# Performance work log

Hardware: AMD Instinct MI355X
Metric: run time of the kernel (lower is better)

Reference implementation:

```python
import jax, jax.numpy as jnp
import numpy as np

NP, NA = 200000, 100000        # paper / author node counts
EW, EC = 300000, 300000        # writes / cites edge counts
HID, H, D = 128, 4, 32         # hidden, heads, head dim
FIN_P, FIN_A, OUT = 256, 128, 16
SCALE = float(1.0 / np.sqrt(D))


def _seg_softmax(alpha, idx, n):
    # softmax over edges grouped by destination node (PyG softmax)
    m = jax.ops.segment_max(alpha, idx, num_segments=n)
    e = jnp.exp(alpha - m[idx])
    s = jax.ops.segment_sum(e, idx, num_segments=n)
    return e / (s[idx] + 1e-16)


def _edge_type(k_src, v_src, q_dst, src, dst, a_rel, m_rel, p_rel, n_dst):
    # per-relation transform at node level, then gather-attend-scatter
    kr = jnp.einsum('nhd,hde->nhe', k_src, a_rel)
    vr = jnp.einsum('nhd,hde->nhe', v_src, m_rel)
    alpha = jnp.sum(q_dst[dst] * kr[src], axis=-1) * p_rel * SCALE  # [E,H]
    alpha = _seg_softmax(alpha, dst, n_dst)
    return jax.ops.segment_sum(vr[src] * alpha[..., None], dst, num_segments=n_dst)


def setup_inputs() -> dict:
    key = jax.random.key(0)
    ks = iter(jax.random.split(key, 48))

    def nrm(shape, s=0.05):
        return jax.random.normal(next(ks), shape, jnp.float32) * s

    inp = dict(
        x_paper=nrm((NP, FIN_P), 1.0),
        x_author=nrm((NA, FIN_A), 1.0),
        writes_src=jax.random.randint(next(ks), (EW,), 0, NA, dtype=jnp.int32),
        writes_dst=jax.random.randint(next(ks), (EW,), 0, NP, dtype=jnp.int32),
        cites_src=jax.random.randint(next(ks), (EC,), 0, NP, dtype=jnp.int32),
        cites_dst=jax.random.randint(next(ks), (EC,), 0, NP, dtype=jnp.int32),
        lin_paper_w=nrm((FIN_P, HID)), lin_paper_b=jnp.zeros((HID,), jnp.float32),
        lin_author_w=nrm((FIN_A, HID)), lin_author_b=jnp.zeros((HID,), jnp.float32),
        lin_out_w=nrm((HID, OUT)), lin_out_b=jnp.zeros((OUT,), jnp.float32),
    )
    for t in ('paper', 'author'):
        for nm in ('k', 'q', 'v', 'a'):
            inp[f'{nm}_w_{t}'] = nrm((HID, HID))
            inp[f'{nm}_b_{t}'] = jnp.zeros((HID,), jnp.float32)
        inp[f'skip_{t}'] = jnp.ones((), jnp.float32)
    for e in ('writes', 'cites'):
        inp[f'a_rel_{e}'] = nrm((H, D, D), 0.18)
        inp[f'm_rel_{e}'] = nrm((H, D, D), 0.18)
        inp[f'p_rel_{e}'] = jnp.ones((H,), jnp.float32)
    return inp


def reference(x_paper, x_author, writes_src, writes_dst, cites_src, cites_dst,
              lin_paper_w, lin_paper_b, lin_author_w, lin_author_b,
              lin_out_w, lin_out_b,
              k_w_paper, k_b_paper, q_w_paper, q_b_paper, v_w_paper, v_b_paper,
              a_w_paper, a_b_paper, skip_paper,
              k_w_author, k_b_author, q_w_author, q_b_author, v_w_author, v_b_author,
              a_w_author, a_b_author, skip_author,
              a_rel_writes, m_rel_writes, p_rel_writes,
              a_rel_cites, m_rel_cites, p_rel_cites):
    # per-node-type input projection + relu
    hp = jax.nn.relu(x_paper @ lin_paper_w + lin_paper_b)
    ha = jax.nn.relu(x_author @ lin_author_w + lin_author_b)
    # HGTConv: per-node-type k/q/v, [N,H,D]
    k_p = (hp @ k_w_paper + k_b_paper).reshape(NP, H, D)
    q_p = (hp @ q_w_paper + q_b_paper).reshape(NP, H, D)
    v_p = (hp @ v_w_paper + v_b_paper).reshape(NP, H, D)
    k_a = (ha @ k_w_author + k_b_author).reshape(NA, H, D)
    v_a = (ha @ v_w_author + v_b_author).reshape(NA, H, D)
    # heterogeneous multi-relation attention, group='sum' over edge types
    out_p = _edge_type(k_a, v_a, q_p, writes_src, writes_dst,
                       a_rel_writes, m_rel_writes, p_rel_writes, NP)
    out_p = out_p + _edge_type(k_p, v_p, q_p, cites_src, cites_dst,
                               a_rel_cites, m_rel_cites, p_rel_cites, NP)
    # output projection + gated skip (paper type; only 'paper' feeds the head)
    op = jax.nn.gelu(out_p.reshape(NP, HID), approximate=False) @ a_w_paper + a_b_paper
    beta = jax.nn.sigmoid(skip_paper)
    hp = beta * op + (1.0 - beta) * hp
    return hp @ lin_out_w + lin_out_b  # [NP, OUT]
```

## Files before the change

kernel.cpp:

```cpp
#include <hip/hip_runtime.h>
#include <cstdint>

#define NP 200000
#define NA 100000
#define EW 300000
#define EC 300000
#define HID 128
#define FIN_P 256
#define FIN_A 128
#define NOUT 16
#define ATT_SCALE 0.17677669529663687f

#define NBP 1563
#define NBA 782

#define SCAN_N (2 * NP)
#define SCAN_BS 256
#define SCAN_ITEMS 4
#define SCAN_TILE 1024
#define SCAN_NB ((SCAN_N + SCAN_TILE - 1) / SCAN_TILE)

typedef short s8v __attribute__((ext_vector_type(8)));
typedef float f32x4 __attribute__((ext_vector_type(4)));
typedef unsigned short ushort_t;

__device__ __forceinline__ float gelu_f(float x) {
  return 0.5f * x * (1.0f + erff(x * 0.70710678118654752f));
}
__device__ __forceinline__ ushort_t f2bf(float f) {
  unsigned u = __float_as_uint(f);
  return (ushort_t)((u + 0x7FFFu + ((u >> 16) & 1u)) >> 16);
}
__device__ __forceinline__ unsigned pack2bf(float a, float b) {
  return (unsigned)f2bf(a) | ((unsigned)f2bf(b) << 16);
}
__device__ __forceinline__ unsigned cvtpk(float a, float b) {
  unsigned r;
  asm("v_cvt_pk_bf16_f32 %0, %1, %2" : "=v"(r) : "v"(a), "v"(b));
  return r;
}
__device__ __forceinline__ float bflo(unsigned u) { return __uint_as_float(u << 16); }
__device__ __forceinline__ float bfhi(unsigned u) { return __uint_as_float(u & 0xFFFF0000u); }

__device__ __forceinline__ void gl16(const void* g, void* l) {
  __builtin_amdgcn_global_load_lds(
      (const __attribute__((address_space(1))) void*)g,
      (__attribute__((address_space(3))) void*)l, 16, 0, 0);
}

__device__ __forceinline__ int s2row(int r) { return (r ^ (r >> 2)) & 3; }

__global__ void prep_all(
    const float* __restrict__ qw,  const float* __restrict__ qb,
    const float* __restrict__ kwp, const float* __restrict__ kbp, const float* __restrict__ arc,
    const float* __restrict__ vwp, const float* __restrict__ vbp, const float* __restrict__ mrc,
    const float* __restrict__ kwa, const float* __restrict__ kba, const float* __restrict__ arw,
    const float* __restrict__ vwa, const float* __restrict__ vba, const float* __restrict__ mrw,
    const float* __restrict__ lpw, const float* __restrict__ law,
    const float* __restrict__ aw, const float* __restrict__ ab,
    const float* __restrict__ skip, const float* __restrict__ W2, const float* __restrict__ b2,
    ushort_t* __restrict__ Wall, float* __restrict__ Ball,
    ushort_t* __restrict__ Wcatb, float* __restrict__ bo,
    int* __restrict__ cnt)
{
  const int b = blockIdx.x, tid = threadIdx.x;
  if (b == 0) {
    for (int idx = tid; idx < 16384; idx += 256) {
      int c = idx >> 7, r = idx & 127;
      Wall[idx] = f2bf(qw[r * 128 + c]);
    }
    for (int c = tid; c < 128; c += 256) Ball[c] = qb[c];
  } else if (b <= 4) {
    const float *W, *bias, *rel;
    switch (b) {
      case 1:  W = kwp; bias = kbp; rel = arc; break;
      case 2:  W = vwp; bias = vbp; rel = mrc; break;
      case 3:  W = kwa; bias = kba; rel = arw; break;
      default: W = vwa; bias = vba; rel = mrw; break;
    }
    for (int idx = tid; idx < 16384; idx += 256) {
      int c = idx >> 7, r = idx & 127, h = c >> 5, e = c & 31;
      float s = 0.f;
      #pragma unroll
      for (int d = 0; d < 32; ++d) s += W[r * 128 + h * 32 + d] * rel[h * 1024 + d * 32 + e];
      Wall[b * 16384 + idx] = f2bf(s);
    }
    for (int c = tid; c < 128; c += 256) {
      int h = c >> 5, e = c & 31;
      float s = 0.f;
      #pragma unroll
      for (int d = 0; d < 32; ++d) s += bias[h * 32 + d] * rel[h * 1024 + d * 32 + e];
      Ball[b * 128 + c] = s;
    }
  } else if (b == 5) {
    for (int idx = tid; idx < 16384; idx += 256) {
      int c = idx >> 7, r = idx & 127;
      Wall[5 * 16384 + idx] = f2bf(law[r * 128 + c]);
    }
  } else if (b == 6) {
    for (int idx = tid; idx < 32768; idx += 256) {
      int c = idx >> 8, r = idx & 255;
      Wall[6 * 16384 + idx] = f2bf(lpw[r * 128 + c]);
    }
  } else if (b == 7) {
    float beta = 1.0f / (1.0f + expf(-skip[0]));
    for (int idx = tid; idx < 4096; idx += 256) {
      int c = idx >> 8, k = idx & 255;
      float v;
      if (k < 128) {
        float s = 0.f;
        for (int j = 0; j < 128; ++j) s += aw[k * 128 + j] * W2[j * 16 + c];
        v = beta * s;
      } else {
        v = (1.0f - beta) * W2[(k - 128) * 16 + c];
      }
      Wcatb[c * 256 + k] = f2bf(v);
    }
    if (tid < 16) {
      float s = 0.f;
      for (int k = 0; k < 128; ++k) s += ab[k] * W2[k * 16 + tid];
      bo[tid] = beta * s + b2[tid];
    }
  } else {
    int chunk = SCAN_N / 8;
    int base = (b - 8) * chunk;
    for (int i = tid; i < chunk; i += 256) cnt[base + i] = 0;
  }
}

__global__ __launch_bounds__(256, 1) void gemm_proj(
    const float* __restrict__ xp, const float* __restrict__ xa,
    const ushort_t* __restrict__ Wall,
    const float* __restrict__ bp, const float* __restrict__ ba,
    ushort_t* __restrict__ hpo, ushort_t* __restrict__ hao)
{
  __shared__ ushort_t As[8192];
  __shared__ ushort_t Bs[8192];
  const bool isP = blockIdx.x < NBP;
  const int bid = isP ? blockIdx.x : blockIdx.x - NBP;
  const float* A = isP ? xp : xa;
  const ushort_t* W = Wall + (isP ? 6 * 16384 : 5 * 16384);
  const float* bias = isP ? bp : ba;
  ushort_t* C = isP ? hpo : hao;
  const int M = isP ? NP : NA;
  const int KT = isP ? 256 : 128;
  const int nt = KT >> 6;

  const int tid  = threadIdx.x;
  const int lane = tid & 63;
  const int wv   = tid >> 6;
  const int wr   = wv >> 1, wc = wv & 1;
  const int l15  = lane & 15, kgl = lane >> 4;
  const int s2l  = (l15 ^ (l15 >> 2)) & 3;
  const int row0 = bid * 128;

  const int r0 = tid >> 2, kgp = tid & 3;
  const int sk = kgp ^ s2row(r0);
  int g0 = row0 + r0;       if (g0 > M - 1) g0 = M - 1;
  int g1 = row0 + r0 + 64;  if (g1 > M - 1) g1 = M - 1;
  const float* a0p = A + (size_t)g0 * KT + sk * 8;
  const float* a1p = A + (size_t)g1 * KT + sk * 8;
  const ushort_t* b0p = W + (size_t)r0 * KT + sk * 8;
  const ushort_t* b1p = W + (size_t)(r0 + 64) * KT + sk * 8;

  f32x4 acc[4][4];
  #pragma unroll
  for (int i = 0; i < 4; ++i)
    #pragma unroll
    for (int j = 0; j < 4; ++j) acc[i][j] = (f32x4){0.f, 0.f, 0.f, 0.f};

  for (int t = 0; t < nt; ++t) {
    const int kt = t * 64;
    gl16(b0p + kt,      &Bs[(size_t)tid * 8]);
    gl16(b1p + kt,      &Bs[(size_t)(tid + 256) * 8]);
    gl16(b0p + kt + 32, &Bs[(size_t)(tid + 512) * 8]);
    gl16(b1p + kt + 32, &Bs[(size_t)(tid + 768) * 8]);
    float4 fa0 = *(const float4*)(a0p + kt);
    float4 fa1 = *(const float4*)(a0p + kt + 4);
    float4 fa2 = *(const float4*)(a1p + kt);
    float4 fa3 = *(const float4*)(a1p + kt + 4);
    float4 fb0 = *(const float4*)(a0p + kt + 32);
    float4 fb1 = *(const float4*)(a0p + kt + 36);
    float4 fb2 = *(const float4*)(a1p + kt + 32);
    float4 fb3 = *(const float4*)(a1p + kt + 36);
    uint4 v;
    v.x = cvtpk(fa0.x, fa0.y); v.y = cvtpk(fa0.z, fa0.w);
    v.z = cvtpk(fa1.x, fa1.y); v.w = cvtpk(fa1.z, fa1.w);
    *(uint4*)&As[(size_t)tid * 8] = v;
    v.x = cvtpk(fa2.x, fa2.y); v.y = cvtpk(fa2.z, fa2.w);
    v.z = cvtpk(fa3.x, fa3.y); v.w = cvtpk(fa3.z, fa3.w);
    *(uint4*)&As[(size_t)(tid + 256) * 8] = v;
    v.x = cvtpk(fb0.x, fb0.y); v.y = cvtpk(fb0.z, fb0.w);
    v.z = cvtpk(fb1.x, fb1.y); v.w = cvtpk(fb1.z, fb1.w);
    *(uint4*)&As[(size_t)(tid + 512) * 8] = v;
    v.x = cvtpk(fb2.x, fb2.y); v.y = cvtpk(fb2.z, fb2.w);
    v.z = cvtpk(fb3.x, fb3.y); v.w = cvtpk(fb3.z, fb3.w);
    *(uint4*)&As[(size_t)(tid + 768) * 8] = v;
    __syncthreads();

    const s8v* As8 = (const s8v*)As;
    const s8v* Bs8 = (const s8v*)Bs;
    #pragma unroll
    for (int pg = 0; pg < 2; ++pg) {
      s8v af[4], bfv[4];
      #pragma unroll
      for (int i = 0; i < 4; ++i)
        af[i]  = As8[pg * 512 + (wr * 64 + i * 16 + l15) * 4 + (kgl ^ s2l)];
      #pragma unroll
      for (int j = 0; j < 4; ++j)
        bfv[j] = Bs8[pg * 512 + (wc * 64 + j * 16 + l15) * 4 + (kgl ^ s2l)];
      #pragma unroll
      for (int i = 0; i < 4; ++i)
        #pragma unroll
        for (int j = 0; j < 4; ++j)
          acc[i][j] = __builtin_amdgcn_mfma_f32_16x16x32_bf16(af[i], bfv[j], acc[i][j], 0, 0, 0);
    }
    __syncthreads();
  }

  float bv[4];
  #pragma unroll
  for (int j = 0; j < 4; ++j) bv[j] = bias[wc * 64 + j * 16 + l15];
  #pragma unroll
  for (int i = 0; i < 4; ++i) {
    #pragma unroll
    for (int r = 0; r < 4; ++r) {
      int row = row0 + wr * 64 + i * 16 + kgl * 4 + r;
      if (row < M) {
        #pragma unroll
        for (int j = 0; j < 4; ++j) {
          float vv = acc[i][j][r] + bv[j];
          vv = fmaxf(vv, 0.f);
          C[(size_t)row * 128 + wc * 64 + j * 16 + l15] = f2bf(vv);
        }
      }
    }
  }
}

__global__ __launch_bounds__(256) void gemm_kv(
    const ushort_t* __restrict__ hpA, const ushort_t* __restrict__ haA,
    const ushort_t* __restrict__ Wall, const float* __restrict__ Ball,
    ushort_t* __restrict__ qkv, ushort_t* __restrict__ kvw)
{
  __shared__ ushort_t As[16384];
  __shared__ ushort_t Bs[16384];
  const bool isP = blockIdx.x < NBP;
  const int bid = isP ? blockIdx.x : blockIdx.x - NBP;
  const ushort_t* A = isP ? hpA : haA;
  const int M = isP ? NP : NA;
  const int base_set = isP ? 0 : 3;
  const int nsets = isP ? 3 : 2;

  const int tid  = threadIdx.x;
  const int lane = tid & 63;
  const int wv   = tid >> 6;
  const int wr   = wv >> 1, wc = wv & 1;
  const int l15  = lane & 15, kgl = lane >> 4;
  const int s2l  = (l15 ^ (l15 >> 2)) & 3;
  const int row0 = bid * 128;

  const int r0 = tid >> 2, kgp = tid & 3;
  const int sk = kgp ^ s2row(r0);
  int g0 = row0 + r0;       if (g0 > M - 1) g0 = M - 1;
  int g1 = row0 + r0 + 64;  if (g1 > M - 1) g1 = M - 1;
  const ushort_t* a0p = A + (size_t)g0 * 128 + sk * 8;
  const ushort_t* a1p = A + (size_t)g1 * 128 + sk * 8;

  #pragma unroll
  for (int t = 0; t < 4; ++t) {
    gl16(a0p + t * 32, &As[((size_t)t * 512 + tid) * 8]);
    gl16(a1p + t * 32, &As[((size_t)t * 512 + tid + 256) * 8]);
  }

  for (int si = 0; si < nsets; ++si) {
    const int set = base_set + si;
    const ushort_t* W = Wall + set * 16384;
    const float* bias = Ball + set * 128;
    ushort_t* C = isP ? (qkv + (size_t)set * NP * HID)
                      : (kvw + (size_t)(set - 3) * NA * HID);
    const ushort_t* b0p = W + (size_t)r0 * 128 + sk * 8;
    const ushort_t* b1p = W + (size_t)(r0 + 64) * 128 + sk * 8;
    #pragma unroll
    for (int t = 0; t < 4; ++t) {
      gl16(b0p + t * 32, &Bs[((size_t)t * 512 + tid) * 8]);
      gl16(b1p + t * 32, &Bs[((size_t)t * 512 + tid + 256) * 8]);
    }
    __syncthreads();

    f32x4 acc[4][4];
    #pragma unroll
    for (int i = 0; i < 4; ++i)
      #pragma unroll
      for (int j = 0; j < 4; ++j) acc[i][j] = (f32x4){0.f, 0.f, 0.f, 0.f};

    const s8v* As8 = (const s8v*)As;
    const s8v* Bs8 = (const s8v*)Bs;
    #pragma unroll
    for (int t = 0; t < 4; ++t) {
      s8v af[4], bfv[4];
      #pragma unroll
      for (int i = 0; i < 4; ++i)
        af[i]  = As8[t * 512 + (wr * 64 + i * 16 + l15) * 4 + (kgl ^ s2l)];
      #pragma unroll
      for (int j = 0; j < 4; ++j)
        bfv[j] = Bs8[t * 512 + (wc * 64 + j * 16 + l15) * 4 + (kgl ^ s2l)];
      #pragma unroll
      for (int i = 0; i < 4; ++i)
        #pragma unroll
        for (int j = 0; j < 4; ++j)
          acc[i][j] = __builtin_amdgcn_mfma_f32_16x16x32_bf16(af[i], bfv[j], acc[i][j], 0, 0, 0);
    }

    float bv[4];
    #pragma unroll
    for (int j = 0; j < 4; ++j) bv[j] = bias[wc * 64 + j * 16 + l15];
    #pragma unroll
    for (int i = 0; i < 4; ++i) {
      #pragma unroll
      for (int r = 0; r < 4; ++r) {
        int row = row0 + wr * 64 + i * 16 + kgl * 4 + r;
        if (row < M) {
          #pragma unroll
          for (int j = 0; j < 4; ++j) {
            C[(size_t)row * 128 + wc * 64 + j * 16 + l15] = f2bf(acc[i][j][r] + bv[j]);
          }
        }
      }
    }
    __syncthreads();
  }
}

__global__ void hist_k(const int* __restrict__ wdst, const int* __restrict__ cdst,
                       int* __restrict__ cnt)
{
  int t = blockIdx.x * blockDim.x + threadIdx.x;
  if (t < EW) atomicAdd(&cnt[wdst[t]], 1);
  if (t < EC) atomicAdd(&cnt[NP + cdst[t]], 1);
}

__global__ __launch_bounds__(SCAN_BS) void scan1(const int* __restrict__ cnt,
                                                 int* __restrict__ off,
                                                 int* __restrict__ bsum)
{
  __shared__ int sh[2][SCAN_BS];
  int tid = threadIdx.x;
  int base = blockIdx.x * SCAN_TILE + tid * SCAN_ITEMS;
  int v[SCAN_ITEMS]; int tsum = 0;
  #pragma unroll
  for (int i = 0; i < SCAN_ITEMS; ++i) {
    int idx = base + i;
    v[i] = (idx < SCAN_N) ? cnt[idx] : 0;
    tsum += v[i];
  }
  int p = 0;
  sh[0][tid] = tsum; __syncthreads();
  #pragma unroll
  for (int d = 1; d < SCAN_BS; d <<= 1) {
    int x = sh[p][tid] + ((tid >= d) ? sh[p][tid - d] : 0);
    sh[p ^ 1][tid] = x; __syncthreads(); p ^= 1;
  }
  int run = sh[p][tid] - tsum;
  #pragma unroll
  for (int i = 0; i < SCAN_ITEMS; ++i) {
    int idx = base + i;
    if (idx < SCAN_N) off[idx] = run;
    run += v[i];
  }
  if (tid == SCAN_BS - 1) bsum[blockIdx.x] = sh[p][tid];
}

__global__ __launch_bounds__(512) void scan2(int* __restrict__ bsum)
{
  __shared__ int sh[2][512];
  int tid = threadIdx.x;
  int v = (tid < SCAN_NB) ? bsum[tid] : 0;
  int p = 0;
  sh[0][tid] = v; __syncthreads();
  for (int d = 1; d < 512; d <<= 1) {
    int x = sh[p][tid] + ((tid >= d) ? sh[p][tid - d] : 0);
    sh[p ^ 1][tid] = x; __syncthreads(); p ^= 1;
  }
  if (tid < SCAN_NB) bsum[tid] = sh[p][tid] - v;
}

__global__ __launch_bounds__(SCAN_BS) void scan3(int* __restrict__ off, int* __restrict__ cur,
                                                 const int* __restrict__ bsum)
{
  int add = bsum[blockIdx.x];
  int base = blockIdx.x * SCAN_TILE + threadIdx.x;
  #pragma unroll
  for (int i = 0; i < SCAN_ITEMS; ++i) {
    int idx = base + i * SCAN_BS;
    if (idx < SCAN_N) { int t = off[idx] + add; off[idx] = t; cur[idx] = t; }
  }
  if (blockIdx.x == 0 && threadIdx.x == 0) off[SCAN_N] = EW + EC;
}

__global__ void fill_k(const int* __restrict__ wsrc, const int* __restrict__ wdst,
                       const int* __restrict__ csrc, const int* __restrict__ cdst,
                       int* __restrict__ cur, int* __restrict__ esrc)
{
  int t = blockIdx.x * blockDim.x + threadIdx.x;
  if (t < EW) { int p = atomicAdd(&cur[wdst[t]], 1); esrc[p] = wsrc[t] << 8; }
  if (t < EC) { int p = atomicAdd(&cur[NP + cdst[t]], 1); esrc[p] = csrc[t] << 8; }
}

__global__ __launch_bounds__(256) void node_attn(
    const int* __restrict__ off, const int* __restrict__ esrc,
    const ushort_t* __restrict__ q,
    const ushort_t* __restrict__ kr_w, const ushort_t* __restrict__ vr_w,
    const ushort_t* __restrict__ kr_c, const ushort_t* __restrict__ vr_c,
    const float* __restrict__ p_rel_w, const float* __restrict__ p_rel_c,
    ushort_t* __restrict__ out_p)
{
  int gid = blockIdx.x * blockDim.x + threadIdx.x;
  int node = gid >> 4;
  int l16 = gid & 15;
  int h = l16 >> 2;
  unsigned loff = (unsigned)(l16 * 16);

  int eb0 = off[node],      ee0 = off[node + 1];
  int eb1 = off[NP + node], ee1 = off[NP + node + 1];

  uint4 qv = *(const uint4*)(q + (size_t)node * HID + l16 * 8);

  int pi0 = (eb0 < ee0) ? eb0 : 0;
  int pi1 = (eb1 < ee1) ? eb1 : 0;
  unsigned pb0 = (unsigned)esrc[pi0] + loff;
  unsigned pb1 = (unsigned)esrc[pi1] + loff;
  uint4 pk[2], pv[2];
  pk[0] = *(const uint4*)((const char*)kr_w + pb0);
  pv[0] = *(const uint4*)((const char*)vr_w + pb0);
  pk[1] = *(const uint4*)((const char*)kr_c + pb1);
  pv[1] = *(const uint4*)((const char*)vr_c + pb1);

  float qf[8];
  {
    const unsigned* pq = (const unsigned*)&qv;
    #pragma unroll
    for (int w = 0; w < 4; ++w) { qf[2 * w] = bflo(pq[w]); qf[2 * w + 1] = bfhi(pq[w]); }
  }
  float prw = p_rel_w[h] * ATT_SCALE;
  float prc = p_rel_c[h] * ATT_SCALE;

  float t[8];
  #pragma unroll
  for (int i = 0; i < 8; ++i) t[i] = 0.f;

  #pragma unroll
  for (int r = 0; r < 2; ++r) {
    const char* krb = (const char*)((r == 0) ? kr_w : kr_c);
    const char* vrb = (const char*)((r == 0) ? vr_w : vr_c);
    float prr = (r == 0) ? prw : prc;
    int eb = (r == 0) ? eb0 : eb1;
    int ee = (r == 0) ? ee0 : ee1;

    float s = 0.f;
    float A[8];
    #pragma unroll
    for (int i = 0; i < 8; ++i) A[i] = 0.f;

    int e = eb;
    if (e < ee) {
      const unsigned* k8 = (const unsigned*)&pk[r];
      const unsigned* v8 = (const unsigned*)&pv[r];
      float d = 0.f;
      #pragma unroll
      for (int w = 0; w < 4; ++w) {
        d = fmaf(qf[2 * w], bflo(k8[w]), d);
        d = fmaf(qf[2 * w + 1], bfhi(k8[w]), d);
      }
      d += __shfl_xor(d, 1);
      d += __shfl_xor(d, 2);
      float p = __expf(d * prr);
      s += p;
      #pragma unroll
      for (int w = 0; w < 4; ++w) {
        A[2 * w]     = fmaf(p, bflo(v8[w]), A[2 * w]);
        A[2 * w + 1] = fmaf(p, bfhi(v8[w]), A[2 * w + 1]);
      }
      ++e;
    }
    for (; e < ee; ++e) {
      unsigned kb = (unsigned)esrc[e] + loff;
      uint4 kv = *(const uint4*)(krb + kb);
      uint4 vv = *(const uint4*)(vrb + kb);
      const unsigned* k8 = (const unsigned*)&kv;
      float d = 0.f;
      #pragma unroll
      for (int w = 0; w < 4; ++w) {
        d = fmaf(qf[2 * w], bflo(k8[w]), d);
        d = fmaf(qf[2 * w + 1], bfhi(k8[w]), d);
      }
      d += __shfl_xor(d, 1);
      d += __shfl_xor(d, 2);
      float p = __expf(d * prr);
      s += p;
      const unsigned* v8 = (const unsigned*)&vv;
      #pragma unroll
      for (int w = 0; w < 4; ++w) {
        A[2 * w]     = fmaf(p, bflo(v8[w]), A[2 * w]);
        A[2 * w + 1] = fmaf(p, bfhi(v8[w]), A[2 * w + 1]);
      }
    }
    float inv = 1.0f / (s + 1e-16f);
    #pragma unroll
    for (int i = 0; i < 8; ++i) t[i] = fmaf(A[i], inv, t[i]);
  }

  uint4 o;
  unsigned* po = (unsigned*)&o;
  #pragma unroll
  for (int w = 0; w < 4; ++w) po[w] = pack2bf(t[2 * w], t[2 * w + 1]);
  *(uint4*)(out_p + (size_t)node * HID + l16 * 8) = o;
}

__global__ __launch_bounds__(256) void epilogue_mfma(
    const ushort_t* __restrict__ out_p, const ushort_t* __restrict__ hp,
    const ushort_t* __restrict__ Wcatb, const float* __restrict__ bo,
    float* __restrict__ out)
{
  __shared__ ushort_t As[4096];
  const int tid  = threadIdx.x;
  const int lane = tid & 63;
  const int wv   = tid >> 6;
  const int l15  = lane & 15, kgl = lane >> 4;
  const int s2l  = (l15 ^ (l15 >> 2)) & 3;
  const int row0 = blockIdx.x * 128;

  const int r0 = tid >> 2, kgp = tid & 3;
  const int sk = kgp ^ s2row(r0);
  int g0 = row0 + r0;       if (g0 > NP - 1) g0 = NP - 1;
  int g1 = row0 + r0 + 64;  if (g1 > NP - 1) g1 = NP - 1;

  s8v bfr[8];
  #pragma unroll
  for (int ks = 0; ks < 8; ++ks)
    bfr[ks] = *(const s8v*)(Wcatb + (size_t)l15 * 256 + ks * 32 + kgl * 8);
  float bo_l = bo[l15];

  f32x4 acc[2];
  acc[0] = (f32x4){0.f, 0.f, 0.f, 0.f};
  acc[1] = (f32x4){0.f, 0.f, 0.f, 0.f};

  #pragma unroll
  for (int ph = 0; ph < 8; ++ph) {
    if (ph < 4) {
      const int kt = ph * 32;
      uint4 v0 = *(const uint4*)(out_p + (size_t)g0 * 128 + kt + sk * 8);
      uint4 v1 = *(const uint4*)(out_p + (size_t)g1 * 128 + kt + sk * 8);
      unsigned* p0 = (unsigned*)&v0;
      unsigned* p1 = (unsigned*)&v1;
      #pragma unroll
      for (int w = 0; w < 4; ++w) {
        p0[w] = cvtpk(gelu_f(bflo(p0[w])), gelu_f(bfhi(p0[w])));
        p1[w] = cvtpk(gelu_f(bflo(p1[w])), gelu_f(bfhi(p1[w])));
      }
      *(uint4*)&As[(size_t)tid * 8] = v0;
      *(uint4*)&As[(size_t)(tid + 256) * 8] = v1;
    } else {
      const int kt = (ph - 4) * 32;
      gl16(hp + (size_t)g0 * 128 + kt + sk * 8, &As[(size_t)tid * 8]);
      gl16(hp + (size_t)g1 * 128 + kt + sk * 8, &As[(size_t)(tid + 256) * 8]);
    }
    __syncthreads();

    const s8v* As8 = (const s8v*)As;
    s8v af0 = As8[(wv * 32 + l15) * 4 + (kgl ^ s2l)];
    s8v af1 = As8[(wv * 32 + 16 + l15) * 4 + (kgl ^ s2l)];
    acc[0] = __builtin_amdgcn_mfma_f32_16x16x32_bf16(af0, bfr[ph], acc[0], 0, 0, 0);
    acc[1] = __builtin_amdgcn_mfma_f32_16x16x32_bf16(af1, bfr[ph], acc[1], 0, 0, 0);
    __syncthreads();
  }

  #pragma unroll
  for (int i = 0; i < 2; ++i) {
    #pragma unroll
    for (int r = 0; r < 4; ++r) {
      int row = row0 + wv * 32 + i * 16 + kgl * 4 + r;
      if (row < NP) out[(size_t)row * NOUT + l15] = acc[i][r] + bo_l;
    }
  }
}

extern "C" void kernel_launch(void* const* d_in, const int* in_sizes, int n_in,
                              void* d_out, int out_size, void* d_ws, size_t ws_size,
                              hipStream_t stream)
{
  (void)in_sizes; (void)n_in; (void)out_size; (void)ws_size;
  const float* x_paper      = (const float*)d_in[0];
  const float* x_author     = (const float*)d_in[1];
  const int*   writes_src   = (const int*)d_in[2];
  const int*   writes_dst   = (const int*)d_in[3];
  const int*   cites_src    = (const int*)d_in[4];
  const int*   cites_dst    = (const int*)d_in[5];
  const float* lin_paper_w  = (const float*)d_in[6];
  const float* lin_paper_b  = (const float*)d_in[7];
  const float* lin_author_w = (const float*)d_in[8];
  const float* lin_author_b = (const float*)d_in[9];
  const float* lin_out_w    = (const float*)d_in[10];
  const float* lin_out_b    = (const float*)d_in[11];
  const float* k_w_paper    = (const float*)d_in[12];
  const float* k_b_paper    = (const float*)d_in[13];
  const float* q_w_paper    = (const float*)d_in[14];
  const float* q_b_paper    = (const float*)d_in[15];
  const float* v_w_paper    = (const float*)d_in[16];
  const float* v_b_paper    = (const float*)d_in[17];
  const float* a_w_paper    = (const float*)d_in[18];
  const float* a_b_paper    = (const float*)d_in[19];
  const float* skip_paper   = (const float*)d_in[20];
  const float* k_w_author   = (const float*)d_in[21];
  const float* k_b_author   = (const float*)d_in[22];
  const float* v_w_author   = (const float*)d_in[25];
  const float* v_b_author   = (const float*)d_in[26];
  const float* a_rel_writes = (const float*)d_in[30];
  const float* m_rel_writes = (const float*)d_in[31];
  const float* p_rel_writes = (const float*)d_in[32];
  const float* a_rel_cites  = (const float*)d_in[33];
  const float* m_rel_cites  = (const float*)d_in[34];
  const float* p_rel_cites  = (const float*)d_in[35];

  float* ws = (float*)d_ws;
  size_t off_f = 0;
  auto nxt = [&](size_t nfloats) { float* p = ws + off_f; off_f += nfloats; return p; };
  ushort_t* hp    = (ushort_t*)nxt((size_t)NP * 64);
  ushort_t* ha    = (ushort_t*)nxt((size_t)NA * 64);
  ushort_t* qkv   = (ushort_t*)nxt((size_t)3 * NP * 64);
  ushort_t* kvw   = (ushort_t*)nxt((size_t)2 * NA * 64);
  ushort_t* outp  = (ushort_t*)nxt((size_t)NP * 64);
  int*      cnt   = (int*)nxt(SCAN_N);
  int*      offs  = (int*)nxt(SCAN_N + 2);
  int*      cur   = (int*)nxt(SCAN_N);
  int*      esrc  = (int*)nxt(EW + EC);
  int*      bsum  = (int*)nxt(512);
  ushort_t* Wall  = (ushort_t*)nxt(65536);
  float*    Ball  = nxt(5 * 128);
  ushort_t* Wcatb = (ushort_t*)nxt(2048);
  float*    bo    = nxt(16);

  ushort_t* q_p  = qkv;
  ushort_t* kr_c = qkv + (size_t)NP * HID;
  ushort_t* vr_c = qkv + (size_t)2 * NP * HID;
  ushort_t* kr_w = kvw;
  ushort_t* vr_w = kvw + (size_t)NA * HID;

  prep_all<<<16, 256, 0, stream>>>(q_w_paper, q_b_paper,
                                   k_w_paper, k_b_paper, a_rel_cites,
                                   v_w_paper, v_b_paper, m_rel_cites,
                                   k_w_author, k_b_author, a_rel_writes,
                                   v_w_author, v_b_author, m_rel_writes,
                                   lin_paper_w, lin_author_w,
                                   a_w_paper, a_b_paper, skip_paper, lin_out_w, lin_out_b,
                                   Wall, Ball, Wcatb, bo, cnt);

  hist_k<<<(300000 + 255) / 256, 256, 0, stream>>>(writes_dst, cites_dst, cnt);
  scan1<<<SCAN_NB, SCAN_BS, 0, stream>>>(cnt, offs, bsum);
  scan2<<<1, 512, 0, stream>>>(bsum);
  scan3<<<SCAN_NB, SCAN_BS, 0, stream>>>(offs, cur, bsum);
  fill_k<<<(300000 + 255) / 256, 256, 0, stream>>>(writes_src, writes_dst,
                                                   cites_src, cites_dst, cur, esrc);

  gemm_proj<<<NBP + NBA, 256, 0, stream>>>(x_paper, x_author, Wall,
                                           lin_paper_b, lin_author_b, hp, ha);
  gemm_kv<<<NBP + NBA, 256, 0, stream>>>(hp, ha, Wall, Ball, qkv, kvw);

  node_attn<<<(NP * 16) / 256, 256, 0, stream>>>(
      offs, esrc, q_p, kr_w, vr_w, kr_c, vr_c, p_rel_writes, p_rel_cites, outp);

  epilogue_mfma<<<NBP, 256, 0, stream>>>(outp, hp, Wcatb, bo, (float*)d_out);
}
```

Before: 386.0 us.

## Fuse input projection and K/Q/V GEMMs into a single kernel

Merges the input-projection GEMM and the K/Q/V GEMM into one kernel. Each block computes its relu projection tile, writes it to global memory, synchronises, then reloads those same rows straight into shared memory for the per-type K/Q/V products. This removes one kernel launch and lets the reload of the hidden rows hit cache instead of HBM. In exchange the first phase now uses the larger shared-memory allocation, and correctness relies on the block's own global writes being visible to its later reads after the barrier.

```diff
diff --git a/kernel.cpp b/kernel.cpp
--- a/kernel.cpp
+++ b/kernel.cpp
@@ -128,23 +128,27 @@
   }
 }
 
-__global__ __launch_bounds__(256, 1) void gemm_proj(
+__global__ __launch_bounds__(256) void gemm_main(
     const float* __restrict__ xp, const float* __restrict__ xa,
     const ushort_t* __restrict__ Wall,
     const float* __restrict__ bp, const float* __restrict__ ba,
-    ushort_t* __restrict__ hpo, ushort_t* __restrict__ hao)
-{
-  __shared__ ushort_t As[8192];
-  __shared__ ushort_t Bs[8192];
+    const float* __restrict__ Ball,
+    ushort_t* __restrict__ hpo, ushort_t* __restrict__ hao,
+    ushort_t* __restrict__ qkv, ushort_t* __restrict__ kvw)
+{
+  __shared__ ushort_t As[16384];
+  __shared__ ushort_t Bs[16384];
   const bool isP = blockIdx.x < NBP;
   const int bid = isP ? blockIdx.x : blockIdx.x - NBP;
   const float* A = isP ? xp : xa;
-  const ushort_t* W = Wall + (isP ? 6 * 16384 : 5 * 16384);
-  const float* bias = isP ? bp : ba;
-  ushort_t* C = isP ? hpo : hao;
+  const ushort_t* Wp = Wall + (isP ? 6 * 16384 : 5 * 16384);
+  const float* biasp = isP ? bp : ba;
+  ushort_t* Chp = isP ? hpo : hao;
   const int M = isP ? NP : NA;
   const int KT = isP ? 256 : 128;
   const int nt = KT >> 6;
+  const int base_set = isP ? 0 : 3;
+  const int nsets = isP ? 3 : 2;
 
   const int tid  = threadIdx.x;
   const int lane = tid & 63;
@@ -158,163 +162,71 @@
   const int sk = kgp ^ s2row(r0);
   int g0 = row0 + r0;       if (g0 > M - 1) g0 = M - 1;
   int g1 = row0 + r0 + 64;  if (g1 > M - 1) g1 = M - 1;
-  const float* a0p = A + (size_t)g0 * KT + sk * 8;
-  const float* a1p = A + (size_t)g1 * KT + sk * 8;
-  const ushort_t* b0p = W + (size_t)r0 * KT + sk * 8;
-  const ushort_t* b1p = W + (size_t)(r0 + 64) * KT + sk * 8;
-
-  f32x4 acc[4][4];
-  #pragma unroll
-  for (int i = 0; i < 4; ++i)
-    #pragma unroll
-    for (int j = 0; j < 4; ++j) acc[i][j] = (f32x4){0.f, 0.f, 0.f, 0.f};
-
-  for (int t = 0; t < nt; ++t) {
-    const int kt = t * 64;
-    gl16(b0p + kt,      &Bs[(size_t)tid * 8]);
-    gl16(b1p + kt,      &Bs[(size_t)(tid + 256) * 8]);
-    gl16(b0p + kt + 32, &Bs[(size_t)(tid + 512) * 8]);
-    gl16(b1p + kt + 32, &Bs[(size_t)(tid + 768) * 8]);
-    float4 fa0 = *(const float4*)(a0p + kt);
-    float4 fa1 = *(const float4*)(a0p + kt + 4);
-    float4 fa2 = *(const float4*)(a1p + kt);
-    float4 fa3 = *(const float4*)(a1p + kt + 4);
-    float4 fb0 = *(const float4*)(a0p + kt + 32);
-    float4 fb1 = *(const float4*)(a0p + kt + 36);
-    float4 fb2 = *(const float4*)(a1p + kt + 32);
-    float4 fb3 = *(const float4*)(a1p + kt + 36);
-    uint4 v;
-    v.x = cvtpk(fa0.x, fa0.y); v.y = cvtpk(fa0.z, fa0.w);
-    v.z = cvtpk(fa1.x, fa1.y); v.w = cvtpk(fa1.z, fa1.w);
-    *(uint4*)&As[(size_t)tid * 8] = v;
-    v.x = cvtpk(fa2.x, fa2.y); v.y = cvtpk(fa2.z, fa2.w);
-    v.z = cvtpk(fa3.x, fa3.y); v.w = cvtpk(fa3.z, fa3.w);
-    *(uint4*)&As[(size_t)(tid + 256) * 8] = v;
-    v.x = cvtpk(fb0.x, fb0.y); v.y = cvtpk(fb0.z, fb0.w);
-    v.z = cvtpk(fb1.x, fb1.y); v.w = cvtpk(fb1.z, fb1.w);
-    *(uint4*)&As[(size_t)(tid + 512) * 8] = v;
-    v.x = cvtpk(fb2.x, fb2.y); v.y = cvtpk(fb2.z, fb2.w);
-    v.z = cvtpk(fb3.x, fb3.y); v.w = cvtpk(fb3.z, fb3.w);
-    *(uint4*)&As[(size_t)(tid + 768) * 8] = v;
-    __syncthreads();
-
-    const s8v* As8 = (const s8v*)As;
-    const s8v* Bs8 = (const s8v*)Bs;
-    #pragma unroll
-    for (int pg = 0; pg < 2; ++pg) {
-      s8v af[4], bfv[4];
-      #pragma unroll
-      for (int i = 0; i < 4; ++i)
-        af[i]  = As8[pg * 512 + (wr * 64 + i * 16 + l15) * 4 + (kgl ^ s2l)];
-      #pragma unroll
-      for (int j = 0; j < 4; ++j)
-        bfv[j] = Bs8[pg * 512 + (wc * 64 + j * 16 + l15) * 4 + (kgl ^ s2l)];
-      #pragma unroll
-      for (int i = 0; i < 4; ++i)
+
+  {
+    const float* a0p = A + (size_t)g0 * KT + sk * 8;
+    const float* a1p = A + (size_t)g1 * KT + sk * 8;
+    const ushort_t* b0p = Wp + (size_t)r0 * KT + sk * 8;
+    const ushort_t* b1p = Wp + (size_t)(r0 + 64) * KT + sk * 8;
+
+    f32x4 acc[4][4];
+    #pragma unroll
+    for (int i = 0; i < 4; ++i)
+      #pragma unroll
+      for (int j = 0; j < 4; ++j) acc[i][j] = (f32x4){0.f, 0.f, 0.f, 0.f};
+
+    for (int t = 0; t < nt; ++t) {
+      const int kt = t * 64;
+      gl16(b0p + kt,      &Bs[(size_t)tid * 8]);
+      gl16(b1p + kt,      &Bs[(size_t)(tid + 256) * 8]);
+      gl16(b0p + kt + 32, &Bs[(size_t)(tid + 512) * 8]);
+      gl16(b1p + kt + 32, &Bs[(size_t)(tid + 768) * 8]);
+      float4 fa0 = *(const float4*)(a0p + kt);
+      float4 fa1 = *(const float4*)(a0p + kt + 4);
+      float4 fa2 = *(const float4*)(a1p + kt);
+      float4 fa3 = *(const float4*)(a1p + kt + 4);
+      float4 fb0 = *(const float4*)(a0p + kt + 32);
+      float4 fb1 = *(const float4*)(a0p + kt + 36);
+      float4 fb2 = *(const float4*)(a1p + kt + 32);
+      float4 fb3 = *(const float4*)(a1p + kt + 36);
+      uint4 v;
+      v.x = cvtpk(fa0.x, fa0.y); v.y = cvtpk(fa0.z, fa0.w);
+      v.z = cvtpk(fa1.x, fa1.y); v.w = cvtpk(fa1.z, fa1.w);
+      *(uint4*)&As[(size_t)tid * 8] = v;
+      v.x = cvtpk(fa2.x, fa2.y); v.y = cvtpk(fa2.z, fa2.w);
+      v.z = cvtpk(fa3.x, fa3.y); v.w = cvtpk(fa3.z, fa3.w);
+      *(uint4*)&As[(size_t)(tid + 256) * 8] = v;
+      v.x = cvtpk(fb0.x, fb0.y); v.y = cvtpk(fb0.z, fb0.w);
+      v.z = cvtpk(fb1.x, fb1.y); v.w = cvtpk(fb1.z, fb1.w);
+      *(uint4*)&As[(size_t)(tid + 512) * 8] = v;
+      v.x = cvtpk(fb2.x, fb2.y); v.y = cvtpk(fb2.z, fb2.w);
+      v.z = cvtpk(fb3.x, fb3.y); v.w = cvtpk(fb3.z, fb3.w);
+      *(uint4*)&As[(size_t)(tid + 768) * 8] = v;
+      __syncthreads();
+
+      const s8v* As8 = (const s8v*)As;
+      const s8v* Bs8 = (const s8v*)Bs;
+      #pragma unroll
+      for (int pg = 0; pg < 2; ++pg) {
+        s8v af[4], bfv[4];
+        #pragma unroll
+        for (int i = 0; i < 4; ++i)
+          af[i]  = As8[pg * 512 + (wr * 64 + i * 16 + l15) * 4 + (kgl ^ s2l)];
         #pragma unroll
         for (int j = 0; j < 4; ++j)
-          acc[i][j] = __builtin_amdgcn_mfma_f32_16x16x32_bf16(af[i], bfv[j], acc[i][j], 0, 0, 0);
-    }
-    __syncthreads();
-  }
-
-  float bv[4];
-  #pragma unroll
-  for (int j = 0; j < 4; ++j) bv[j] = bias[wc * 64 + j * 16 + l15];
-  #pragma unroll
-  for (int i = 0; i < 4; ++i) {
-    #pragma unroll
-    for (int r = 0; r < 4; ++r) {
-      int row = row0 + wr * 64 + i * 16 + kgl * 4 + r;
-      if (row < M) {
-        #pragma unroll
-        for (int j = 0; j < 4; ++j) {
-          float vv = acc[i][j][r] + bv[j];
-          vv = fmaxf(vv, 0.f);
-          C[(size_t)row * 128 + wc * 64 + j * 16 + l15] = f2bf(vv);
-        }
-      }
-    }
-  }
-}
-
-__global__ __launch_bounds__(256) void gemm_kv(
-    const ushort_t* __restrict__ hpA, const ushort_t* __restrict__ haA,
-    const ushort_t* __restrict__ Wall, const float* __restrict__ Ball,
-    ushort_t* __restrict__ qkv, ushort_t* __restrict__ kvw)
-{
-  __shared__ ushort_t As[16384];
-  __shared__ ushort_t Bs[16384];
-  const bool isP = blockIdx.x < NBP;
-  const int bid = isP ? blockIdx.x : blockIdx.x - NBP;
-  const ushort_t* A = isP ? hpA : haA;
-  const int M = isP ? NP : NA;
-  const int base_set = isP ? 0 : 3;
-  const int nsets = isP ? 3 : 2;
-
-  const int tid  = threadIdx.x;
-  const int lane = tid & 63;
-  const int wv   = tid >> 6;
-  const int wr   = wv >> 1, wc = wv & 1;
-  const int l15  = lane & 15, kgl = lane >> 4;
-  const int s2l  = (l15 ^ (l15 >> 2)) & 3;
-  const int row0 = bid * 128;
-
-  const int r0 = tid >> 2, kgp = tid & 3;
-  const int sk = kgp ^ s2row(r0);
-  int g0 = row0 + r0;       if (g0 > M - 1) g0 = M - 1;
-  int g1 = row0 + r0 + 64;  if (g1 > M - 1) g1 = M - 1;
-  const ushort_t* a0p = A + (size_t)g0 * 128 + sk * 8;
-  const ushort_t* a1p = A + (size_t)g1 * 128 + sk * 8;
-
-  #pragma unroll
-  for (int t = 0; t < 4; ++t) {
-    gl16(a0p + t * 32, &As[((size_t)t * 512 + tid) * 8]);
-    gl16(a1p + t * 32, &As[((size_t)t * 512 + tid + 256) * 8]);
-  }
-
-  for (int si = 0; si < nsets; ++si) {
-    const int set = base_set + si;
-    const ushort_t* W = Wall + set * 16384;
-    const float* bias = Ball + set * 128;
-    ushort_t* C = isP ? (qkv + (size_t)set * NP * HID)
-                      : (kvw + (size_t)(set - 3) * NA * HID);
-    const ushort_t* b0p = W + (size_t)r0 * 128 + sk * 8;
-    const ushort_t* b1p = W + (size_t)(r0 + 64) * 128 + sk * 8;
-    #pragma unroll
-    for (int t = 0; t < 4; ++t) {
-      gl16(b0p + t * 32, &Bs[((size_t)t * 512 + tid) * 8]);
-      gl16(b1p + t * 32, &Bs[((size_t)t * 512 + tid + 256) * 8]);
-    }
-    __syncthreads();
-
-    f32x4 acc[4][4];
-    #pragma unroll
-    for (int i = 0; i < 4; ++i)
-      #pragma unroll
-      for (int j = 0; j < 4; ++j) acc[i][j] = (f32x4){0.f, 0.f, 0.f, 0.f};
-
-    const s8v* As8 = (const s8v*)As;
-    const s8v* Bs8 = (const s8v*)Bs;
-    #pragma unroll
-    for (int t = 0; t < 4; ++t) {
-      s8v af[4], bfv[4];
-      #pragma unroll
-      for (int i = 0; i < 4; ++i)
-        af[i]  = As8[t * 512 + (wr * 64 + i * 16 + l15) * 4 + (kgl ^ s2l)];
-      #pragma unroll
-      for (int j = 0; j < 4; ++j)
-        bfv[j] = Bs8[t * 512 + (wc * 64 + j * 16 + l15) * 4 + (kgl ^ s2l)];
-      #pragma unroll
-      for (int i = 0; i < 4; ++i)
-        #pragma unroll
-        for (int j = 0; j < 4; ++j)
-          acc[i][j] = __builtin_amdgcn_mfma_f32_16x16x32_bf16(af[i], bfv[j], acc[i][j], 0, 0, 0);
+          bfv[j] = Bs8[pg * 512 + (wc * 64 + j * 16 + l15) * 4 + (kgl ^ s2l)];
+        #pragma unroll
+        for (int i = 0; i < 4; ++i)
+          #pragma unroll
+          for (int j = 0; j < 4; ++j)
+            acc[i][j] = __builtin_amdgcn_mfma_f32_16x16x32_bf16(af[i], bfv[j], acc[i][j], 0, 0, 0);
+      }
+      __syncthreads();
     }
 
     float bv[4];
     #pragma unroll
-    for (int j = 0; j < 4; ++j) bv[j] = bias[wc * 64 + j * 16 + l15];
+    for (int j = 0; j < 4; ++j) bv[j] = biasp[wc * 64 + j * 16 + l15];
     #pragma unroll
     for (int i = 0; i < 4; ++i) {
       #pragma unroll
@@ -323,12 +235,82 @@
         if (row < M) {
           #pragma unroll
           for (int j = 0; j < 4; ++j) {
-            C[(size_t)row * 128 + wc * 64 + j * 16 + l15] = f2bf(acc[i][j][r] + bv[j]);
+            float vv = acc[i][j][r] + bv[j];
+            vv = fmaxf(vv, 0.f);
+            Chp[(size_t)row * 128 + wc * 64 + j * 16 + l15] = f2bf(vv);
           }
         }
       }
     }
-    __syncthreads();
+  }
+  __syncthreads();
+
+  {
+    const ushort_t* a0h = Chp + (size_t)g0 * 128 + sk * 8;
+    const ushort_t* a1h = Chp + (size_t)g1 * 128 + sk * 8;
+    #pragma unroll
+    for (int t = 0; t < 4; ++t) {
+      gl16(a0h + t * 32, &As[((size_t)t * 512 + tid) * 8]);
+      gl16(a1h + t * 32, &As[((size_t)t * 512 + tid + 256) * 8]);
+    }
+
+    for (int si = 0; si < nsets; ++si) {
+      const int set = base_set + si;
+      const ushort_t* W = Wall + set * 16384;
+      const float* bias = Ball + set * 128;
+      ushort_t* C = isP ? (qkv + (size_t)set * NP * HID)
+                        : (kvw + (size_t)(set - 3) * NA * HID);
+      const ushort_t* b0p = W + (size_t)r0 * 128 + sk * 8;
+      const ushort_t* b1p = W + (size_t)(r0 + 64) * 128 + sk * 8;
+      #pragma unroll
+      for (int t = 0; t < 4; ++t) {
+        gl16(b0p + t * 32, &Bs[((size_t)t * 512 + tid) * 8]);
+        gl16(b1p + t * 32, &Bs[((size_t)t * 512 + tid + 256) * 8]);
+      }
+      __syncthreads();
+
+      f32x4 acc[4][4];
+      #pragma unroll
+      for (int i = 0; i < 4; ++i)
+        #pragma unroll
+        for (int j = 0; j < 4; ++j) acc[i][j] = (f32x4){0.f, 0.f, 0.f, 0.f};
+
+      const s8v* As8 = (const s8v*)As;
+      const s8v* Bs8 = (const s8v*)Bs;
+      #pragma unroll
+      for (int t = 0; t < 4; ++t) {
+        s8v af[4], bfv[4];
+        #pragma unroll
+        for (int i = 0; i < 4; ++i)
+          af[i]  = As8[t * 512 + (wr * 64 + i * 16 + l15) * 4 + (kgl ^ s2l)];
+        #pragma unroll
+        for (int j = 0; j < 4; ++j)
+          bfv[j] = Bs8[t * 512 + (wc * 64 + j * 16 + l15) * 4 + (kgl ^ s2l)];
+        #pragma unroll
+        for (int i = 0; i < 4; ++i)
+          #pragma unroll
+          for (int j = 0; j < 4; ++j)
+            acc[i][j] = __builtin_amdgcn_mfma_f32_16x16x32_bf16(af[i], bfv[j], acc[i][j], 0, 0, 0);
+      }
+
+      float bv[4];
+      #pragma unroll
+      for (int j = 0; j < 4; ++j) bv[j] = bias[wc * 64 + j * 16 + l15];
+      #pragma unroll
+      for (int i = 0; i < 4; ++i) {
+        #pragma unroll
+        for (int r = 0; r < 4; ++r) {
+          int row = row0 + wr * 64 + i * 16 + kgl * 4 + r;
+          if (row < M) {
+            #pragma unroll
+            for (int j = 0; j < 4; ++j) {
+              C[(size_t)row * 128 + wc * 64 + j * 16 + l15] = f2bf(acc[i][j][r] + bv[j]);
+            }
+          }
+        }
+      }
+      __syncthreads();
+    }
   }
 }
 
@@ -662,9 +644,9 @@
   fill_k<<<(300000 + 255) / 256, 256, 0, stream>>>(writes_src, writes_dst,
                                                    cites_src, cites_dst, cur, esrc);
 
-  gemm_proj<<<NBP + NBA, 256, 0, stream>>>(x_paper, x_author, Wall,
-                                           lin_paper_b, lin_author_b, hp, ha);
-  gemm_kv<<<NBP + NBA, 256, 0, stream>>>(hp, ha, Wall, Ball, qkv, kvw);
+  gemm_main<<<NBP + NBA, 256, 0, stream>>>(x_paper, x_author, Wall,
+                                           lin_paper_b, lin_author_b, Ball,
+                                           hp, ha, qkv, kvw);
 
   node_attn<<<(NP * 16) / 256, 256, 0, stream>>>(
       offs, esrc, q_p, kr_w, vr_w, kr_c, vr_c, p_rel_writes, p_rel_cites, outp);
```

Result: no change. 385.4 us (-0.1%).
